# Optimization experiments

Measured on AMD Instinct MI355X. Metric: run time of the kernel, lower is better.

The kernel has to match this reference:

```python
import jax, jax.numpy as jnp
import numpy as np

LN_EPS = 1e-5


def setup_inputs() -> dict:
    key = jax.random.key(0)
    ks = jax.random.split(key, 4)
    B, S, D, V, M = 32, 512, 1024, 32000, 77
    X = jax.random.normal(ks[0], (B, S, D), dtype=jnp.float32)
    masked_positions = jax.random.randint(ks[1], (B, M), 0, S, dtype=jnp.int64 if jax.config.jax_enable_x64 else jnp.int32)
    W1 = jax.random.normal(ks[2], (D, D), dtype=jnp.float32) * (1.0 / np.sqrt(D))
    b1 = jnp.zeros((D,), jnp.float32)
    gamma = jnp.ones((D,), jnp.float32)
    beta = jnp.zeros((D,), jnp.float32)
    W2 = jax.random.normal(ks[3], (D, V), dtype=jnp.float32) * (1.0 / np.sqrt(D))
    b2 = jnp.zeros((V,), jnp.float32)
    return {"X": X, "masked_positions": masked_positions, "W1": W1, "b1": b1,
            "gamma": gamma, "beta": beta, "W2": W2, "b2": b2}


def reference(X, masked_positions, W1, b1, gamma, beta, W2, b2):
    # Gather masked token embeddings: X[b, masked_positions[b, m]] -> [B, M, D]
    masked_X = jnp.take_along_axis(X, masked_positions[:, :, None], axis=1)
    # Linear -> ReLU
    h = jax.nn.relu(jnp.einsum('bmd,dh->bmh', masked_X, W1) + b1)
    # LayerNorm over last dim
    mu = jnp.mean(h, axis=-1, keepdims=True)
    var = jnp.mean(jnp.square(h - mu), axis=-1, keepdims=True)
    h = (h - mu) * jax.lax.rsqrt(var + LN_EPS) * gamma + beta
    # Vocab projection
    return jnp.einsum('bmh,hv->bmv', h, W2) + b2
```

## Files before the change

### kernel.cpp

```cpp
#include <hip/hip_runtime.h>
#include <cstdint>

#define D_DIM 1024
#define V_DIM 32000
#define S_DIM 512
#define M_TOK 77
#define ROWS 2464
#define ROWS_PAD 2560

#define G2_BM 256
#define G2_BN 256
#define G2_BK 32
#define G2_MT (ROWS_PAD / G2_BM)
#define G2_NT (V_DIM / G2_BN)
#define G2_NWG (G2_MT * G2_NT)
#define G2_KT (D_DIM / G2_BK)

typedef __attribute__((ext_vector_type(8))) short bf16x8;
typedef __attribute__((ext_vector_type(4))) float f32x4;
typedef __attribute__((ext_vector_type(4))) uint16_t u16x4;

__device__ __forceinline__ uint16_t f2bf(float f) {
    union { float f; uint32_t u; } w; w.f = f;
    uint32_t r = (w.u + 0x7FFFu + ((w.u >> 16) & 1u)) >> 16;
    return (uint16_t)r;
}

__device__ __forceinline__ void async_copy16(const uint16_t* g, uint16_t* l) {
    __builtin_amdgcn_global_load_lds((const __attribute__((address_space(1))) void*)g,
                                     (__attribute__((address_space(3))) void*)l,
                                     16, 0, 0);
}

__global__ __launch_bounds__(256) void transpose_f32_bf16(const float* __restrict__ in,
                                                          uint16_t* __restrict__ out,
                                                          int R, int C) {
    __shared__ uint16_t tile[64][65];
    const int c0 = blockIdx.x * 64, r0 = blockIdx.y * 64;
    const int t  = threadIdx.x;
    const int lr = t >> 4;
    const int lc = (t & 15) * 4;
#pragma unroll
    for (int p = 0; p < 4; ++p) {
        const float* src = in + (size_t)(r0 + p * 16 + lr) * C + c0 + lc;
        f32x4 v = *(const f32x4*)src;
        tile[p * 16 + lr][lc + 0] = f2bf(v.x);
        tile[p * 16 + lr][lc + 1] = f2bf(v.y);
        tile[p * 16 + lr][lc + 2] = f2bf(v.z);
        tile[p * 16 + lr][lc + 3] = f2bf(v.w);
    }
    __syncthreads();
#pragma unroll
    for (int p = 0; p < 4; ++p) {
        const int oc = p * 16 + lr;
        u16x4 v;
        v.x = tile[lc + 0][oc];
        v.y = tile[lc + 1][oc];
        v.z = tile[lc + 2][oc];
        v.w = tile[lc + 3][oc];
        *(u16x4*)(out + (size_t)(c0 + oc) * R + r0 + lc) = v;
    }
}

__global__ __launch_bounds__(256) void gather_rows(const float* __restrict__ X,
                                                   const int* __restrict__ pos,
                                                   uint16_t* __restrict__ Ag) {
    const int r = blockIdx.x;
    const int t = threadIdx.x;
    size_t src = 0;
    if (r < ROWS) {
        const int b = r / M_TOK;
        const int p = pos[r];
        src = ((size_t)b * S_DIM + p) * D_DIM;
    }
    f32x4 v = *(const f32x4*)(X + src + t * 4);
    u16x4 o;
    o.x = f2bf(v.x); o.y = f2bf(v.y); o.z = f2bf(v.z); o.w = f2bf(v.w);
    *(u16x4*)(Ag + (size_t)r * D_DIM + t * 4) = o;
}

template <int EPI>
__global__ __launch_bounds__(256, 2) void gemm_bt(const uint16_t* __restrict__ A,
                                                  const uint16_t* __restrict__ B,
                                                  const float* __restrict__ bias,
                                                  float* __restrict__ C,
                                                  int K, int N, int MValid) {
    __shared__ uint16_t As[128 * 64];
    __shared__ uint16_t Bs[128 * 64];
    const int tid  = threadIdx.x;
    const int lane = tid & 63;
    const int wave = tid >> 6;
    const int wr   = (wave >> 1) * 64;
    const int wc   = (wave & 1) * 64;
    const int tM   = blockIdx.y * 128;
    const int tN   = blockIdx.x * 128;
    const int l15  = lane & 15;
    const int l4   = lane >> 4;

    const f32x4 zero = {0.f, 0.f, 0.f, 0.f};
    f32x4 acc[4][4];
#pragma unroll
    for (int i = 0; i < 4; ++i)
#pragma unroll
        for (int j = 0; j < 4; ++j) acc[i][j] = zero;

    const uint16_t* Agp = A + (size_t)(tM + (tid >> 3)) * K + (tid & 7) * 8;
    const uint16_t* Bgp = B + (size_t)(tN + (tid >> 3)) * K + (tid & 7) * 8;
    uint16_t* Asl = &As[tid * 8];
    uint16_t* Bsl = &Bs[tid * 8];
    const size_t rstep = (size_t)32 * K;

    for (int k0 = 0; k0 < K; k0 += 64) {
#pragma unroll
        for (int i = 0; i < 4; ++i)
            async_copy16(Agp + i * rstep + k0, Asl + i * 2048);
#pragma unroll
        for (int i = 0; i < 4; ++i)
            async_copy16(Bgp + i * rstep + k0, Bsl + i * 2048);
        __syncthreads();
#pragma unroll
        for (int kk = 0; kk < 2; ++kk) {
            bf16x8 af[4], bfr[4];
#pragma unroll
            for (int i = 0; i < 4; ++i)
                af[i] = *(const bf16x8*)&As[(wr + i * 16 + l15) * 64 + kk * 32 + l4 * 8];
#pragma unroll
            for (int j = 0; j < 4; ++j)
                bfr[j] = *(const bf16x8*)&Bs[(wc + j * 16 + l15) * 64 + kk * 32 + l4 * 8];
#pragma unroll
            for (int i = 0; i < 4; ++i)
#pragma unroll
                for (int j = 0; j < 4; ++j)
                    acc[i][j] = __builtin_amdgcn_mfma_f32_16x16x32_bf16(af[i], bfr[j],
                                                                        acc[i][j], 0, 0, 0);
        }
        __syncthreads();
    }

#pragma unroll
    for (int j = 0; j < 4; ++j) {
        const int col = tN + wc + j * 16 + l15;
        const float bv = bias[col];
#pragma unroll
        for (int i = 0; i < 4; ++i) {
            const int row0 = tM + wr + i * 16 + l4 * 4;
#pragma unroll
            for (int r = 0; r < 4; ++r) {
                const int row = row0 + r;
                float v = acc[i][j][r] + bv;
                if (EPI == 0) {
                    v = v > 0.f ? v : 0.f;
                    C[(size_t)row * N + col] = v;
                } else {
                    if (row < MValid)
                        C[(size_t)row * N + col] = v;
                }
            }
        }
    }
}

#define G2_TILE(T, STAGE, VM)                                                              \
    do {                                                                                   \
        asm volatile("s_waitcnt vmcnt(" #VM ")" ::: "memory");                             \
        __builtin_amdgcn_s_barrier();                                                      \
        const int bufc = ((T) & 3) * 16384;                                                \
        bf16x8 af[4], bfv[4];                                                              \
        _Pragma("unroll") for (int i = 0; i < 4; ++i)                                      \
            af[i] = *(const bf16x8*)&lds[bufc + (R0 + i * 16 + l15) * 32 + swr];           \
        _Pragma("unroll") for (int j = 0; j < 4; ++j)                                      \
            bfv[j] = *(const bf16x8*)&lds[bufc + 8192 + (C0 + j * 16 + l15) * 32 + swr];   \
        if (STAGE) {                                                                       \
            const int sb = (((T) + 3) & 3) * 16384;                                        \
            const int k0 = ((T) + 3) * G2_BK;                                              \
            async_copy16(Ag0 + k0, AsD + sb);                                              \
            async_copy16(Ag1 + k0, AsD + sb + 4096);                                       \
            async_copy16(Bg0 + k0, BsD + sb);                                              \
            async_copy16(Bg1 + k0, BsD + sb + 4096);                                       \
        }                                                                                  \
        __builtin_amdgcn_s_barrier();                                                      \
        asm volatile("s_waitcnt lgkmcnt(0)" ::: "memory");                                 \
        __builtin_amdgcn_s_setprio(1);                                                     \
        _Pragma("unroll") for (int i = 0; i < 4; ++i)                                      \
            _Pragma("unroll") for (int j = 0; j < 4; ++j)                                  \
                acc[i][j] = __builtin_amdgcn_mfma_f32_16x16x32_bf16(af[i], bfv[j],         \
                                                                    acc[i][j], 0, 0, 0);   \
        __builtin_amdgcn_s_setprio(0);                                                     \
        __builtin_amdgcn_s_barrier();                                                      \
        _Pragma("unroll") for (int i = 0; i < 4; ++i)                                      \
            af[i] = *(const bf16x8*)&lds[bufc + (R0 + 64 + i * 16 + l15) * 32 + swr];      \
        __builtin_amdgcn_s_barrier();                                                      \
        asm volatile("s_waitcnt lgkmcnt(0)" ::: "memory");                                 \
        __builtin_amdgcn_s_setprio(1);                                                     \
        _Pragma("unroll") for (int i = 0; i < 4; ++i)                                      \
            _Pragma("unroll") for (int j = 0; j < 4; ++j)                                  \
                acc[4 + i][j] = __builtin_amdgcn_mfma_f32_16x16x32_bf16(af[i], bfv[j],     \
                                                                        acc[4 + i][j],    \
                                                                        0, 0, 0);          \
        __builtin_amdgcn_s_setprio(0);                                                     \
    } while (0)

__global__ __launch_bounds__(512, 2) void gemm2_256(const uint16_t* __restrict__ A,
                                                    const uint16_t* __restrict__ B,
                                                    const float* __restrict__ bias,
                                                    float* __restrict__ C,
                                                    int MValid) {
    __shared__ uint16_t lds[65536];
    const int tid  = threadIdx.x;
    const int lane = tid & 63;
    const int wave = tid >> 6;
    const int l15  = lane & 15;
    const int l4   = lane >> 4;
    const int R0   = (wave >> 2) * 128;
    const int C0   = (wave & 3) * 64;

    const int bid = blockIdx.x;
    const int q = G2_NWG >> 3, r = G2_NWG & 7;
    const int xcd = bid & 7, lin = bid >> 3;
    const int wg = (xcd < r ? xcd * (q + 1) : r * (q + 1) + (xcd - r) * q) + lin;
    const int tM = (wg % G2_MT) * G2_BM;
    const int tN = (wg / G2_MT) * G2_BN;

    const int srow  = tid >> 2;
    const int sslot = tid & 3;
    const int swcol = ((sslot ^ ((srow >> 1) & 3)) << 3);
    const uint16_t* Ag0 = A + (size_t)(tM + srow) * D_DIM + swcol;
    const uint16_t* Ag1 = Ag0 + (size_t)128 * D_DIM;
    const uint16_t* Bg0 = B + (size_t)(tN + srow) * D_DIM + swcol;
    const uint16_t* Bg1 = Bg0 + (size_t)128 * D_DIM;
    uint16_t* AsD = &lds[tid * 8];
    uint16_t* BsD = &lds[8192 + tid * 8];

    const int swr = ((l4 ^ ((l15 >> 1) & 3)) << 3);

    const f32x4 zero = {0.f, 0.f, 0.f, 0.f};
    f32x4 acc[8][4];
#pragma unroll
    for (int i = 0; i < 8; ++i)
#pragma unroll
        for (int j = 0; j < 4; ++j) acc[i][j] = zero;

#pragma unroll
    for (int t = 0; t < 3; ++t) {
        const int sb = t * 16384;
        const int k0 = t * G2_BK;
        async_copy16(Ag0 + k0, AsD + sb);
        async_copy16(Ag1 + k0, AsD + sb + 4096);
        async_copy16(Bg0 + k0, BsD + sb);
        async_copy16(Bg1 + k0, BsD + sb + 4096);
    }

#pragma unroll 2
    for (int T = 0; T < G2_KT - 3; ++T) {
        G2_TILE(T, true, 8);
    }
    G2_TILE(G2_KT - 3, false, 8);
    G2_TILE(G2_KT - 2, false, 4);
    G2_TILE(G2_KT - 1, false, 0);

#pragma unroll
    for (int j = 0; j < 4; ++j) {
        const int col = tN + C0 + j * 16 + l15;
        const float bv = bias[col];
#pragma unroll
        for (int i = 0; i < 8; ++i) {
            const int row0 = tM + R0 + i * 16 + l4 * 4;
#pragma unroll
            for (int rr = 0; rr < 4; ++rr) {
                const int row = row0 + rr;
                if (row < MValid)
                    C[(size_t)row * V_DIM + col] = acc[i][j][rr] + bv;
            }
        }
    }
}

__global__ __launch_bounds__(256) void layernorm_rows(const float* __restrict__ H,
                                                      const float* __restrict__ gamma,
                                                      const float* __restrict__ beta,
                                                      uint16_t* __restrict__ Hn) {
    const int row = blockIdx.x;
    const int t   = threadIdx.x;
    const float* h = H + (size_t)row * D_DIM;
    f32x4 v = *(const f32x4*)(h + t * 4);
    float s  = v.x + v.y + v.z + v.w;
    float sq = v.x * v.x + v.y * v.y + v.z * v.z + v.w * v.w;
#pragma unroll
    for (int o = 32; o > 0; o >>= 1) {
        s  += __shfl_down(s, o, 64);
        sq += __shfl_down(sq, o, 64);
    }
    __shared__ float ss[4], sqs[4];
    if ((t & 63) == 0) { ss[t >> 6] = s; sqs[t >> 6] = sq; }
    __syncthreads();
    const float S    = ss[0] + ss[1] + ss[2] + ss[3];
    const float SQ   = sqs[0] + sqs[1] + sqs[2] + sqs[3];
    const float mean = S * (1.f / D_DIM);
    const float var  = SQ * (1.f / D_DIM) - mean * mean;
    const float rstd = rsqrtf(var + 1e-5f);
    const int c = t * 4;
    f32x4 g = *(const f32x4*)(gamma + c);
    f32x4 bt = *(const f32x4*)(beta + c);
    u16x4 o;
    o.x = f2bf((v.x - mean) * rstd * g.x + bt.x);
    o.y = f2bf((v.y - mean) * rstd * g.y + bt.y);
    o.z = f2bf((v.z - mean) * rstd * g.z + bt.z);
    o.w = f2bf((v.w - mean) * rstd * g.w + bt.w);
    *(u16x4*)(Hn + (size_t)row * D_DIM + c) = o;
}

extern "C" void kernel_launch(void* const* d_in, const int* in_sizes, int n_in,
                              void* d_out, int out_size, void* d_ws, size_t ws_size,
                              hipStream_t stream) {
    const float* X     = (const float*)d_in[0];
    const int*   mp    = (const int*)d_in[1];
    const float* W1    = (const float*)d_in[2];
    const float* b1    = (const float*)d_in[3];
    const float* gamma = (const float*)d_in[4];
    const float* beta  = (const float*)d_in[5];
    const float* W2    = (const float*)d_in[6];
    const float* b2    = (const float*)d_in[7];

    char* ws = (char*)d_ws;
    uint16_t* W2T = (uint16_t*)(ws);
    uint16_t* W1T = (uint16_t*)(ws + 65536000);
    uint16_t* Ag  = (uint16_t*)(ws + 65536000 + 2097152);
    uint16_t* Hn  = (uint16_t*)(ws + 65536000 + 2097152 + 5242880);
    float*    H   = (float*)   (ws + 65536000 + 2097152 + 5242880 + 5242880);

    transpose_f32_bf16<<<dim3(V_DIM / 64, D_DIM / 64), 256, 0, stream>>>(W2, W2T, D_DIM, V_DIM);
    transpose_f32_bf16<<<dim3(D_DIM / 64, D_DIM / 64), 256, 0, stream>>>(W1, W1T, D_DIM, D_DIM);
    gather_rows<<<ROWS_PAD, 256, 0, stream>>>(X, mp, Ag);
    gemm_bt<0><<<dim3(D_DIM / 128, ROWS_PAD / 128), 256, 0, stream>>>(Ag, W1T, b1, H,
                                                                      D_DIM, D_DIM, ROWS_PAD);
    layernorm_rows<<<ROWS_PAD, 256, 0, stream>>>(H, gamma, beta, Hn);
    gemm2_256<<<dim3(G2_NWG), 512, 0, stream>>>(Hn, W2T, b2, (float*)d_out, ROWS);
}
```

Baseline: 693.3 us.

## Software-pipeline LDS fragment reads one K-tile ahead with a single barrier per tile

Restructures the bf16 vocab GEMM main loop so the A and B fragments for the next K-tile are read from LDS right after the current tile's MFMAs are issued. Each tile now needs one wait-plus-barrier, down from four barriers and two explicit lgkmcnt waits. Global-to-LDS staging stays four buffers deep, and the loop unroll goes from 2 to 4. The aim is to hide LDS read latency behind matrix-core work and cut barrier stalls. The cost is holding a full tile of fragments (12 bf16x8 vectors) in registers at once, which raises register pressure and the risk of spills under the 512-thread, 2-block launch bound.

Result: faster. 677.9 us (-2.2%).

```diff
diff --git a/kernel.cpp b/kernel.cpp
--- a/kernel.cpp
+++ b/kernel.cpp
@@ -160,44 +160,44 @@
     }
 }
 
-#define G2_TILE(T, STAGE, VM)                                                              \
+#define G2_SEAM(VM)                                                  \
+    asm volatile("s_waitcnt vmcnt(" #VM ")" ::: "memory");           \
+    __builtin_amdgcn_s_barrier();
+
+#define G2_STAGE(T)                                                  \
+    do {                                                             \
+        const int sb_ = ((T) & 3) * 16384;                           \
+        const int k0_ = (T) * G2_BK;                                 \
+        async_copy16(Ag0 + k0_, AsD + sb_);                          \
+        async_copy16(Ag1 + k0_, AsD + sb_ + 4096);                   \
+        async_copy16(Bg0 + k0_, BsD + sb_);                          \
+        async_copy16(Bg1 + k0_, BsD + sb_ + 4096);                   \
+    } while (0)
+
+#define G2_MFMA()                                                                          \
     do {                                                                                   \
-        asm volatile("s_waitcnt vmcnt(" #VM ")" ::: "memory");                             \
-        __builtin_amdgcn_s_barrier();                                                      \
-        const int bufc = ((T) & 3) * 16384;                                                \
-        bf16x8 af[4], bfv[4];                                                              \
-        _Pragma("unroll") for (int i = 0; i < 4; ++i)                                      \
-            af[i] = *(const bf16x8*)&lds[bufc + (R0 + i * 16 + l15) * 32 + swr];           \
-        _Pragma("unroll") for (int j = 0; j < 4; ++j)                                      \
-            bfv[j] = *(const bf16x8*)&lds[bufc + 8192 + (C0 + j * 16 + l15) * 32 + swr];   \
-        if (STAGE) {                                                                       \
-            const int sb = (((T) + 3) & 3) * 16384;                                        \
-            const int k0 = ((T) + 3) * G2_BK;                                              \
-            async_copy16(Ag0 + k0, AsD + sb);                                              \
-            async_copy16(Ag1 + k0, AsD + sb + 4096);                                       \
-            async_copy16(Bg0 + k0, BsD + sb);                                              \
-            async_copy16(Bg1 + k0, BsD + sb + 4096);                                       \
-        }                                                                                  \
-        __builtin_amdgcn_s_barrier();                                                      \
-        asm volatile("s_waitcnt lgkmcnt(0)" ::: "memory");                                 \
         __builtin_amdgcn_s_setprio(1);                                                     \
         _Pragma("unroll") for (int i = 0; i < 4; ++i)                                      \
             _Pragma("unroll") for (int j = 0; j < 4; ++j)                                  \
-                acc[i][j] = __builtin_amdgcn_mfma_f32_16x16x32_bf16(af[i], bfv[j],         \
+                acc[i][j] = __builtin_amdgcn_mfma_f32_16x16x32_bf16(fa0[i], fb[j],         \
                                                                     acc[i][j], 0, 0, 0);   \
-        __builtin_amdgcn_s_setprio(0);                                                     \
-        __builtin_amdgcn_s_barrier();                                                      \
-        _Pragma("unroll") for (int i = 0; i < 4; ++i)                                      \
-            af[i] = *(const bf16x8*)&lds[bufc + (R0 + 64 + i * 16 + l15) * 32 + swr];      \
-        __builtin_amdgcn_s_barrier();                                                      \
-        asm volatile("s_waitcnt lgkmcnt(0)" ::: "memory");                                 \
-        __builtin_amdgcn_s_setprio(1);                                                     \
         _Pragma("unroll") for (int i = 0; i < 4; ++i)                                      \
             _Pragma("unroll") for (int j = 0; j < 4; ++j)                                  \
-                acc[4 + i][j] = __builtin_amdgcn_mfma_f32_16x16x32_bf16(af[i], bfv[j],     \
-                                                                        acc[4 + i][j],    \
+                acc[4 + i][j] = __builtin_amdgcn_mfma_f32_16x16x32_bf16(fa1[i], fb[j],     \
+                                                                        acc[4 + i][j],     \
                                                                         0, 0, 0);          \
         __builtin_amdgcn_s_setprio(0);                                                     \
+    } while (0)
+
+#define G2_READS(T)                                                                        \
+    do {                                                                                   \
+        const int bufc_ = ((T) & 3) * 16384;                                               \
+        _Pragma("unroll") for (int i = 0; i < 4; ++i)                                      \
+            fa0[i] = *(const bf16x8*)&lds[bufc_ + (R0 + i * 16 + l15) * 32 + swr];         \
+        _Pragma("unroll") for (int i = 0; i < 4; ++i)                                      \
+            fa1[i] = *(const bf16x8*)&lds[bufc_ + (R0 + 64 + i * 16 + l15) * 32 + swr];    \
+        _Pragma("unroll") for (int j = 0; j < 4; ++j)                                      \
+            fb[j] = *(const bf16x8*)&lds[bufc_ + 8192 + (C0 + j * 16 + l15) * 32 + swr];   \
     } while (0)
 
 __global__ __launch_bounds__(512, 2) void gemm2_256(const uint16_t* __restrict__ A,
@@ -240,6 +240,8 @@
 #pragma unroll
         for (int j = 0; j < 4; ++j) acc[i][j] = zero;
 
+    bf16x8 fa0[4], fa1[4], fb[4];
+
 #pragma unroll
     for (int t = 0; t < 3; ++t) {
         const int sb = t * 16384;
@@ -249,14 +251,23 @@
         async_copy16(Bg0 + k0, BsD + sb);
         async_copy16(Bg1 + k0, BsD + sb + 4096);
     }
-
-#pragma unroll 2
+    G2_SEAM(8);
+    G2_READS(0);
+
+#pragma unroll 4
     for (int T = 0; T < G2_KT - 3; ++T) {
-        G2_TILE(T, true, 8);
-    }
-    G2_TILE(G2_KT - 3, false, 8);
-    G2_TILE(G2_KT - 2, false, 4);
-    G2_TILE(G2_KT - 1, false, 0);
+        G2_SEAM(4);
+        G2_STAGE(T + 3);
+        G2_MFMA();
+        G2_READS(T + 1);
+    }
+    G2_SEAM(4);
+    G2_MFMA();
+    G2_READS(30);
+    G2_SEAM(0);
+    G2_MFMA();
+    G2_READS(31);
+    G2_MFMA();
 
 #pragma unroll
     for (int j = 0; j < 4; ++j) {
```
